# Kernel optimization log

Hardware: AMD Instinct MI355X
Metric: run time of the kernel (lower is better)

## Reference

```python
import jax, jax.numpy as jnp
import numpy as np

EMA_ALPHA = 0.1


def setup_inputs() -> dict:
    key = jax.random.key(0)
    k1, k2, k3 = jax.random.split(key, 3)
    B, N, D = 4, 128, 4096
    T, K = 32768, 8
    memory = jax.random.normal(k1, (B, N, D), dtype=jnp.float32)
    hidden_states = jax.random.normal(k2, (T, D), dtype=jnp.float32)
    slot_indices = jax.random.randint(k3, (T, K), 0, N, dtype=jnp.int64)
    return {
        "memory": memory,
        "hidden_states": hidden_states,
        "slot_indices": slot_indices,
        "batch_idx": 1,
    }


def reference(memory, hidden_states, slot_indices, batch_idx):
    # memory: [B, N, D]; hidden_states: [T, D]; slot_indices: [T, K] int
    N = memory.shape[1]
    # Token t touches slot n if ANY of its top-K indices equals n
    # (mirrors torch (slot_indices == idx).any(dim=-1); duplicates in K count once)
    touch = (slot_indices[..., None] == jnp.arange(N)).any(axis=1)  # [T, N] bool
    m = touch.astype(hidden_states.dtype)                           # [T, N]
    counts = m.sum(axis=0)                                          # [N]
    sums = jnp.einsum("tn,td->nd", m, hidden_states)                # [N, D]
    agg = sums / jnp.maximum(counts, 1.0)[:, None]                  # masked mean per slot
    cur = memory[batch_idx]                                         # [N, D]
    upd = EMA_ALPHA * agg + (1.0 - EMA_ALPHA) * cur
    new_row = jnp.where((counts > 0)[:, None], upd, cur)            # untouched slots unchanged
    return memory.at[batch_idx].set(new_row)
```

## Files before the change

kernel.cpp:

```cpp
#include <hip/hip_runtime.h>
#include <hip/hip_bf16.h>

#define T_TOK   32768
#define N_SLOTS 128
#define D_DIM   4096
#define B_DIM   4

#define NCHUNK  16
#define CTOK    (T_TOK / NCHUNK)
#define KB      64
#define NT      (CTOK / KB)
#define WCOLS   128
#define NSLICE  (D_DIM / WCOLS)
#define THREADS 256

typedef __attribute__((ext_vector_type(8))) short short8;
typedef __attribute__((ext_vector_type(4))) float f32x4;

#define PARTIAL_BYTES ((size_t)NCHUNK * N_SLOTS * D_DIM * 4)
#define COUNTS_OFF    PARTIAL_BYTES

#define BAR_LGKM() do { \
    asm volatile("s_waitcnt lgkmcnt(0)" ::: "memory"); \
    __builtin_amdgcn_s_barrier(); \
  } while (0)

__device__ __forceinline__ unsigned int pack_bf2(float lo, float hi) {
  unsigned short a = __bfloat16_as_ushort(__float2bfloat16(lo));
  unsigned short b = __bfloat16_as_ushort(__float2bfloat16(hi));
  return (unsigned int)a | ((unsigned int)b << 16);
}

__global__ __launch_bounds__(256) void prep_kernel(const int* __restrict__ sidx,
                                                   int* __restrict__ counts) {
  __shared__ int cnt[N_SLOTS];
  const int tid = threadIdx.x;
  if (tid < N_SLOTS) cnt[tid] = 0;
  __syncthreads();

  const int t = blockIdx.x * 256 + tid;
  const int4 a = ((const int4*)sidx)[2 * t];
  const int4 b = ((const int4*)sidx)[2 * t + 1];
  int idx[8] = {a.x, a.y, a.z, a.w, b.x, b.y, b.z, b.w};

  #pragma unroll
  for (int k = 0; k < 8; ++k) {
    int n = idx[k];
    bool dup = false;
    #pragma unroll
    for (int j = 0; j < 8; ++j)
      if (j < k) dup |= (idx[j] == n);
    if (!dup && (unsigned)n < (unsigned)N_SLOTS) atomicAdd(&cnt[n], 1);
  }
  __syncthreads();
  if (tid < N_SLOTS && cnt[tid] > 0) atomicAdd(&counts[tid], cnt[tid]);
}

__global__ __launch_bounds__(THREADS, 2) void sums_kernel(
    const float* __restrict__ hidden, const int* __restrict__ sidx,
    float* __restrict__ partial) {
  __shared__ unsigned int   h_w[2][4096];
  __shared__ unsigned short m_u[2][8192];

  const int tid = threadIdx.x;
  const int slice = blockIdx.x & (NSLICE - 1);
  const int chunk = blockIdx.x / NSLICE;
  const int d0 = slice * WCOLS;
  const int cb = chunk * CTOK;

  const int kp = tid & 31;
  const int cg = tid >> 5;

  const int lane = tid & 63;
  const int wv   = tid >> 6;
  const int l15  = lane & 15;
  const int lk   = lane >> 4;

  f32x4 acc[8][2];
  #pragma unroll
  for (int i = 0; i < 8; ++i)
    #pragma unroll
    for (int j = 0; j < 2; ++j)
      acc[i][j] = (f32x4){0.f, 0.f, 0.f, 0.f};

  float4 fa[4], fb[4];
  int s0, s1;

  {
    const float* hp = hidden + (size_t)(cb + 2 * kp) * D_DIM + d0 + cg * 16;
    #pragma unroll
    for (int q = 0; q < 4; ++q) {
      fa[q] = ((const float4*)hp)[q];
      fb[q] = ((const float4*)(hp + D_DIM))[q];
    }
    s0 = sidx[cb * 8 + tid];
    s1 = sidx[cb * 8 + 256 + tid];
  }

  for (int t = 0; t < NT; ++t) {
    const int b = t & 1;
    const int cs0 = s0, cs1 = s1;

    #pragma unroll
    for (int q = 0; q < 4; ++q) {
      const int colbase = cg * 16 + q * 4;
      const float ax[4] = {fa[q].x, fa[q].y, fa[q].z, fa[q].w};
      const float bx[4] = {fb[q].x, fb[q].y, fb[q].z, fb[q].w};
      #pragma unroll
      for (int c = 0; c < 4; ++c) {
        const int col = colbase + c;
        h_w[b][col * 32 + (kp ^ ((col & 7) << 2))] = pack_bf2(ax[c], bx[c]);
      }
    }

    if (t + 1 < NT) {
      const int tb = cb + (t + 1) * KB;
      const float* hp = hidden + (size_t)(tb + 2 * kp) * D_DIM + d0 + cg * 16;
      #pragma unroll
      for (int q = 0; q < 4; ++q) {
        fa[q] = ((const float4*)hp)[q];
        fb[q] = ((const float4*)(hp + D_DIM))[q];
      }
      s0 = sidx[tb * 8 + tid];
      s1 = sidx[tb * 8 + 256 + tid];
    }

    {
      uint4* mz = (uint4*)m_u[b];
      const uint4 z = make_uint4(0, 0, 0, 0);
      #pragma unroll
      for (int i = 0; i < 4; ++i) mz[i * THREADS + tid] = z;
    }
    BAR_LGKM();

    {
      const int n0 = cs0 & (N_SLOTS - 1);
      const int t0 = tid >> 3;
      m_u[b][n0 * 64 + (t0 ^ ((n0 & 7) << 3))] = 0x3F80;
      const int n1 = cs1 & (N_SLOTS - 1);
      const int t1 = (tid + 256) >> 3;
      m_u[b][n1 * 64 + (t1 ^ ((n1 & 7) << 3))] = 0x3F80;
    }
    BAR_LGKM();

    {
      const unsigned short* mb = m_u[b];
      const unsigned short* hb = (const unsigned short*)h_w[b];
      #pragma unroll
      for (int ks = 0; ks < 2; ++ks) {
        const int kbase = ks * 32 + lk * 8;
        const int col0 = (wv * 2) * 16 + l15;
        const int col1 = (wv * 2 + 1) * 16 + l15;
        const short8 bf0 = *(const short8*)&hb[col0 * 64 + (kbase ^ ((col0 & 7) << 3))];
        const short8 bf1 = *(const short8*)&hb[col1 * 64 + (kbase ^ ((col1 & 7) << 3))];
        #pragma unroll
        for (int mt = 0; mt < 8; ++mt) {
          const int row = mt * 16 + l15;
          const short8 af = *(const short8*)&mb[row * 64 + (kbase ^ ((row & 7) << 3))];
          acc[mt][0] = __builtin_amdgcn_mfma_f32_16x16x32_bf16(af, bf0, acc[mt][0], 0, 0, 0);
          acc[mt][1] = __builtin_amdgcn_mfma_f32_16x16x32_bf16(af, bf1, acc[mt][1], 0, 0, 0);
        }
      }
    }
  }

  float* pbase = partial + (size_t)chunk * N_SLOTS * D_DIM;
  #pragma unroll
  for (int mt = 0; mt < 8; ++mt)
    #pragma unroll
    for (int j = 0; j < 2; ++j) {
      const int col = d0 + (wv * 2 + j) * 16 + l15;
      #pragma unroll
      for (int r = 0; r < 4; ++r) {
        const int row = mt * 16 + lk * 4 + r;
        pbase[(size_t)row * D_DIM + col] = acc[mt][j][r];
      }
    }
}

__global__ __launch_bounds__(256) void final_kernel(const float* __restrict__ memory,
                                                    const float* __restrict__ partial,
                                                    const int* __restrict__ counts,
                                                    const int* __restrict__ bidx_p,
                                                    float* __restrict__ out) {
  const size_t i = (size_t)blockIdx.x * 256 + threadIdx.x;
  float4 v = ((const float4*)memory)[i];
  const size_t rowLen4 = (size_t)N_SLOTS * (D_DIM / 4);
  const size_t rowStart = (size_t)(*bidx_p) * rowLen4;
  if (i >= rowStart && i < rowStart + rowLen4) {
    const size_t rel = i - rowStart;
    const int n  = (int)(rel / (D_DIM / 4));
    const int d4 = (int)(rel % (D_DIM / 4));
    const int c = counts[n];
    if (c > 0) {
      const float4* p4 = (const float4*)partial;
      float4 s = {0.f, 0.f, 0.f, 0.f};
      #pragma unroll
      for (int ch = 0; ch < NCHUNK; ++ch) {
        float4 p = p4[((size_t)ch * N_SLOTS + n) * (D_DIM / 4) + d4];
        s.x += p.x; s.y += p.y; s.z += p.z; s.w += p.w;
      }
      const float w = 0.1f / (float)c;
      v.x = s.x * w + 0.9f * v.x;
      v.y = s.y * w + 0.9f * v.y;
      v.z = s.z * w + 0.9f * v.z;
      v.w = s.w * w + 0.9f * v.w;
    }
  }
  ((float4*)out)[i] = v;
}

extern "C" void kernel_launch(void* const* d_in, const int* in_sizes, int n_in,
                              void* d_out, int out_size, void* d_ws, size_t ws_size,
                              hipStream_t stream) {
  const float* memory = (const float*)d_in[0];
  const float* hidden = (const float*)d_in[1];
  const int*   sidx   = (const int*)d_in[2];
  const int*   bidx   = (const int*)d_in[3];
  float* out = (float*)d_out;

  char* ws = (char*)d_ws;
  float* partial = (float*)ws;
  int*   counts  = (int*)(ws + COUNTS_OFF);

  hipMemsetAsync(counts, 0, 512, stream);

  prep_kernel<<<T_TOK / 256, 256, 0, stream>>>(sidx, counts);

  sums_kernel<<<NCHUNK * NSLICE, THREADS, 0, stream>>>(hidden, sidx, partial);

  const int totalVec4 = B_DIM * N_SLOTS * (D_DIM / 4);
  final_kernel<<<totalVec4 / 256, 256, 0, stream>>>(memory, partial, counts, bidx, out);
}
```

Baseline: 131.7 us.

## Precompute per-token slot bitmaps and build MFMA mask operands in registers

The prep kernel now also writes a 128-bit slot bitmap per token. The sums kernel reads these bitmaps instead of scattering one-hot masks into a zeroed shared-memory matrix, and builds the bf16 mask fragments directly in registers with shifts. This removes one barrier, the mask zeroing and the scatter stores per k-tile. Column slices are halved to 64 columns with more blocks and an occupancy hint of 4, which trades fewer accumulators per thread for more per-lane bit manipulation ALU work and an extra bitmap round trip through global memory.

```diff
diff --git a/kernel.cpp b/kernel.cpp
--- a/kernel.cpp
+++ b/kernel.cpp
@@ -7,18 +7,20 @@
 #define B_DIM   4
 
 #define NCHUNK  16
+#define NSLICE  64
+#define WCOLS   (D_DIM / NSLICE)
 #define CTOK    (T_TOK / NCHUNK)
 #define KB      64
 #define NT      (CTOK / KB)
-#define WCOLS   128
-#define NSLICE  (D_DIM / WCOLS)
 #define THREADS 256
 
+typedef unsigned long long u64;
 typedef __attribute__((ext_vector_type(8))) short short8;
 typedef __attribute__((ext_vector_type(4))) float f32x4;
 
 #define PARTIAL_BYTES ((size_t)NCHUNK * N_SLOTS * D_DIM * 4)
 #define COUNTS_OFF    PARTIAL_BYTES
+#define BITMAP_OFF    (PARTIAL_BYTES + 1024)
 
 #define BAR_LGKM() do { \
     asm volatile("s_waitcnt lgkmcnt(0)" ::: "memory"); \
@@ -32,7 +34,8 @@
 }
 
 __global__ __launch_bounds__(256) void prep_kernel(const int* __restrict__ sidx,
-                                                   int* __restrict__ counts) {
+                                                   int* __restrict__ counts,
+                                                   u64* __restrict__ bitmap) {
   __shared__ int cnt[N_SLOTS];
   const int tid = threadIdx.x;
   if (tid < N_SLOTS) cnt[tid] = 0;
@@ -43,24 +46,29 @@
   const int4 b = ((const int4*)sidx)[2 * t + 1];
   int idx[8] = {a.x, a.y, a.z, a.w, b.x, b.y, b.z, b.w};
 
+  u64 lo = 0, hi = 0;
   #pragma unroll
   for (int k = 0; k < 8; ++k) {
-    int n = idx[k];
+    int n = idx[k] & (N_SLOTS - 1);
+    if (n < 64) lo |= 1ull << n; else hi |= 1ull << (n - 64);
     bool dup = false;
     #pragma unroll
     for (int j = 0; j < 8; ++j)
-      if (j < k) dup |= (idx[j] == n);
-    if (!dup && (unsigned)n < (unsigned)N_SLOTS) atomicAdd(&cnt[n], 1);
-  }
+      if (j < k) dup |= (idx[j] == idx[k]);
+    if (!dup) atomicAdd(&cnt[n], 1);
+  }
+  bitmap[2 * t]     = lo;
+  bitmap[2 * t + 1] = hi;
+
   __syncthreads();
   if (tid < N_SLOTS && cnt[tid] > 0) atomicAdd(&counts[tid], cnt[tid]);
 }
 
-__global__ __launch_bounds__(THREADS, 2) void sums_kernel(
-    const float* __restrict__ hidden, const int* __restrict__ sidx,
+__global__ __launch_bounds__(THREADS, 4) void sums_kernel(
+    const float* __restrict__ hidden, const u64* __restrict__ bitmap,
     float* __restrict__ partial) {
-  __shared__ unsigned int   h_w[2][4096];
-  __shared__ unsigned short m_u[2][8192];
+  __shared__ unsigned int h_w[2][WCOLS * 32];
+  __shared__ __align__(16) u64 mb_w[2][128];
 
   const int tid = threadIdx.x;
   const int slice = blockIdx.x & (NSLICE - 1);
@@ -76,105 +84,93 @@
   const int l15  = lane & 15;
   const int lk   = lane >> 4;
 
-  f32x4 acc[8][2];
+  f32x4 acc[8];
   #pragma unroll
-  for (int i = 0; i < 8; ++i)
-    #pragma unroll
-    for (int j = 0; j < 2; ++j)
-      acc[i][j] = (f32x4){0.f, 0.f, 0.f, 0.f};
-
-  float4 fa[4], fb[4];
-  int s0, s1;
+  for (int mt = 0; mt < 8; ++mt) acc[mt] = (f32x4){0.f, 0.f, 0.f, 0.f};
+
+  float4 fa[2], fb[2];
+  u64 mreg = 0;
 
   {
-    const float* hp = hidden + (size_t)(cb + 2 * kp) * D_DIM + d0 + cg * 16;
-    #pragma unroll
-    for (int q = 0; q < 4; ++q) {
-      fa[q] = ((const float4*)hp)[q];
-      fb[q] = ((const float4*)(hp + D_DIM))[q];
-    }
-    s0 = sidx[cb * 8 + tid];
-    s1 = sidx[cb * 8 + 256 + tid];
+    const float* hp = hidden + (size_t)(cb + 2 * kp) * D_DIM + d0 + cg * 8;
+    fa[0] = ((const float4*)hp)[0];          fa[1] = ((const float4*)hp)[1];
+    fb[0] = ((const float4*)(hp + D_DIM))[0]; fb[1] = ((const float4*)(hp + D_DIM))[1];
+    if (tid < 128) mreg = bitmap[(size_t)cb * 2 + tid];
   }
 
   for (int t = 0; t < NT; ++t) {
     const int b = t & 1;
-    const int cs0 = s0, cs1 = s1;
-
-    #pragma unroll
-    for (int q = 0; q < 4; ++q) {
-      const int colbase = cg * 16 + q * 4;
+
+    #pragma unroll
+    for (int q = 0; q < 2; ++q) {
       const float ax[4] = {fa[q].x, fa[q].y, fa[q].z, fa[q].w};
       const float bx[4] = {fb[q].x, fb[q].y, fb[q].z, fb[q].w};
       #pragma unroll
       for (int c = 0; c < 4; ++c) {
-        const int col = colbase + c;
+        const int col = cg * 8 + q * 4 + c;
         h_w[b][col * 32 + (kp ^ ((col & 7) << 2))] = pack_bf2(ax[c], bx[c]);
       }
     }
+    if (tid < 128) mb_w[b][((tid & 1) << 6) | (tid >> 1)] = mreg;
 
     if (t + 1 < NT) {
       const int tb = cb + (t + 1) * KB;
-      const float* hp = hidden + (size_t)(tb + 2 * kp) * D_DIM + d0 + cg * 16;
-      #pragma unroll
-      for (int q = 0; q < 4; ++q) {
-        fa[q] = ((const float4*)hp)[q];
-        fb[q] = ((const float4*)(hp + D_DIM))[q];
-      }
-      s0 = sidx[tb * 8 + tid];
-      s1 = sidx[tb * 8 + 256 + tid];
-    }
-
-    {
-      uint4* mz = (uint4*)m_u[b];
-      const uint4 z = make_uint4(0, 0, 0, 0);
-      #pragma unroll
-      for (int i = 0; i < 4; ++i) mz[i * THREADS + tid] = z;
-    }
+      const float* hp = hidden + (size_t)(tb + 2 * kp) * D_DIM + d0 + cg * 8;
+      fa[0] = ((const float4*)hp)[0];          fa[1] = ((const float4*)hp)[1];
+      fb[0] = ((const float4*)(hp + D_DIM))[0]; fb[1] = ((const float4*)(hp + D_DIM))[1];
+      if (tid < 128) mreg = bitmap[(size_t)tb * 2 + tid];
+    }
+
     BAR_LGKM();
 
-    {
-      const int n0 = cs0 & (N_SLOTS - 1);
-      const int t0 = tid >> 3;
-      m_u[b][n0 * 64 + (t0 ^ ((n0 & 7) << 3))] = 0x3F80;
-      const int n1 = cs1 & (N_SLOTS - 1);
-      const int t1 = (tid + 256) >> 3;
-      m_u[b][n1 * 64 + (t1 ^ ((n1 & 7) << 3))] = 0x3F80;
-    }
-    BAR_LGKM();
-
-    {
-      const unsigned short* mb = m_u[b];
-      const unsigned short* hb = (const unsigned short*)h_w[b];
-      #pragma unroll
-      for (int ks = 0; ks < 2; ++ks) {
-        const int kbase = ks * 32 + lk * 8;
-        const int col0 = (wv * 2) * 16 + l15;
-        const int col1 = (wv * 2 + 1) * 16 + l15;
-        const short8 bf0 = *(const short8*)&hb[col0 * 64 + (kbase ^ ((col0 & 7) << 3))];
-        const short8 bf1 = *(const short8*)&hb[col1 * 64 + (kbase ^ ((col1 & 7) << 3))];
+    const unsigned short* hb = (const unsigned short*)h_w[b];
+    #pragma unroll
+    for (int ks = 0; ks < 2; ++ks) {
+      const int kbase = ks * 32 + lk * 8;
+      const int col = wv * 16 + l15;
+      const short8 bf = *(const short8*)&hb[col * 64 + (kbase ^ ((col & 7) << 3))];
+
+      u64 w0[8], w1[8];
+      #pragma unroll
+      for (int g = 0; g < 4; ++g) {
+        const ulonglong2 r0 = *(const ulonglong2*)&mb_w[b][kbase + 2 * g];
+        w0[2 * g] = r0.x; w0[2 * g + 1] = r0.y;
+        const ulonglong2 r1 = *(const ulonglong2*)&mb_w[b][64 + kbase + 2 * g];
+        w1[2 * g] = r1.x; w1[2 * g + 1] = r1.y;
+      }
+      unsigned int a0[8], a1[8], c0[8], c1[8];
+      #pragma unroll
+      for (int j = 0; j < 8; ++j) {
+        const u64 s0 = w0[j] >> l15;
+        a0[j] = (unsigned int)s0; a1[j] = (unsigned int)(s0 >> 32);
+        const u64 s1 = w1[j] >> l15;
+        c0[j] = (unsigned int)s1; c1[j] = (unsigned int)(s1 >> 32);
+      }
+      #pragma unroll
+      for (int mt = 0; mt < 8; ++mt) {
+        const unsigned int* src = (mt < 4) ? ((mt & 2) ? a1 : a0)
+                                           : ((mt & 2) ? c1 : c0);
+        const int sh = (mt & 1) * 16;
+        union { unsigned int u[4]; short8 s; } cv;
         #pragma unroll
-        for (int mt = 0; mt < 8; ++mt) {
-          const int row = mt * 16 + l15;
-          const short8 af = *(const short8*)&mb[row * 64 + (kbase ^ ((row & 7) << 3))];
-          acc[mt][0] = __builtin_amdgcn_mfma_f32_16x16x32_bf16(af, bf0, acc[mt][0], 0, 0, 0);
-          acc[mt][1] = __builtin_amdgcn_mfma_f32_16x16x32_bf16(af, bf1, acc[mt][1], 0, 0, 0);
+        for (int p = 0; p < 4; ++p) {
+          const unsigned int b0 = (src[2 * p]     >> sh) & 1u;
+          const unsigned int b1 = (src[2 * p + 1] >> sh) & 1u;
+          cv.u[p] = (b0 | (b1 << 16)) * 0x3F80u;
         }
+        acc[mt] = __builtin_amdgcn_mfma_f32_16x16x32_bf16(cv.s, bf, acc[mt], 0, 0, 0);
       }
     }
   }
 
   float* pbase = partial + (size_t)chunk * N_SLOTS * D_DIM;
+  const int col = d0 + wv * 16 + l15;
   #pragma unroll
   for (int mt = 0; mt < 8; ++mt)
     #pragma unroll
-    for (int j = 0; j < 2; ++j) {
-      const int col = d0 + (wv * 2 + j) * 16 + l15;
-      #pragma unroll
-      for (int r = 0; r < 4; ++r) {
-        const int row = mt * 16 + lk * 4 + r;
-        pbase[(size_t)row * D_DIM + col] = acc[mt][j][r];
-      }
+    for (int r = 0; r < 4; ++r) {
+      const int row = mt * 16 + lk * 4 + r;
+      pbase[(size_t)row * D_DIM + col] = acc[mt][r];
     }
 }
 
@@ -222,12 +218,13 @@
   char* ws = (char*)d_ws;
   float* partial = (float*)ws;
   int*   counts  = (int*)(ws + COUNTS_OFF);
+  u64*   bitmap  = (u64*)(ws + BITMAP_OFF);
 
   hipMemsetAsync(counts, 0, 512, stream);
 
-  prep_kernel<<<T_TOK / 256, 256, 0, stream>>>(sidx, counts);
-
-  sums_kernel<<<NCHUNK * NSLICE, THREADS, 0, stream>>>(hidden, sidx, partial);
+  prep_kernel<<<T_TOK / 256, 256, 0, stream>>>(sidx, counts, bitmap);
+
+  sums_kernel<<<NCHUNK * NSLICE, THREADS, 0, stream>>>(hidden, bitmap, partial);
 
   const int totalVec4 = B_DIM * N_SLOTS * (D_DIM / 4);
   final_kernel<<<totalVec4 / 256, 256, 0, stream>>>(memory, partial, counts, bidx, out);
```

New measurement: 151.4 us. +15.0%, slower.

## Shrink sums-kernel tiles to 64 columns and 32-token steps for higher occupancy

Applied to the files above, without the earlier changes.

The sums kernel now splits D into 64 slices of 64 columns and steps through 32 tokens per iteration, so it launches twice as many blocks. Launch bounds now ask for 4 blocks per CU, and each thread holds 8 accumulators instead of 16. The XOR-swizzled shared layout is replaced by padded rows (stride 40 bf16) to avoid bank conflicts. This is meant to raise occupancy and parallelism. In exchange there are twice as many barrier iterations per chunk, less MFMA work between barriers, and the mask tile is rebuilt twice as often relative to compute.

```diff
diff --git a/kernel.cpp b/kernel.cpp
--- a/kernel.cpp
+++ b/kernel.cpp
@@ -7,13 +7,15 @@
 #define B_DIM   4
 
 #define NCHUNK  16
+#define NSLICE  64
+#define WCOLS   (D_DIM / NSLICE)
 #define CTOK    (T_TOK / NCHUNK)
-#define KB      64
+#define KB      32
 #define NT      (CTOK / KB)
-#define WCOLS   128
-#define NSLICE  (D_DIM / WCOLS)
 #define THREADS 256
-
+#define PADK    40
+
+typedef unsigned long long u64;
 typedef __attribute__((ext_vector_type(8))) short short8;
 typedef __attribute__((ext_vector_type(4))) float f32x4;
 
@@ -25,10 +27,8 @@
     __builtin_amdgcn_s_barrier(); \
   } while (0)
 
-__device__ __forceinline__ unsigned int pack_bf2(float lo, float hi) {
-  unsigned short a = __bfloat16_as_ushort(__float2bfloat16(lo));
-  unsigned short b = __bfloat16_as_ushort(__float2bfloat16(hi));
-  return (unsigned int)a | ((unsigned int)b << 16);
+__device__ __forceinline__ unsigned short bf16u(float x) {
+  return __bfloat16_as_ushort(__float2bfloat16(x));
 }
 
 __global__ __launch_bounds__(256) void prep_kernel(const int* __restrict__ sidx,
@@ -56,19 +56,19 @@
   if (tid < N_SLOTS && cnt[tid] > 0) atomicAdd(&counts[tid], cnt[tid]);
 }
 
-__global__ __launch_bounds__(THREADS, 2) void sums_kernel(
+__global__ __launch_bounds__(THREADS, 4) void sums_kernel(
     const float* __restrict__ hidden, const int* __restrict__ sidx,
     float* __restrict__ partial) {
-  __shared__ unsigned int   h_w[2][4096];
-  __shared__ unsigned short m_u[2][8192];
+  __shared__ __align__(16) unsigned short h_u[2][WCOLS * PADK];
+  __shared__ __align__(16) unsigned short m_u[2][N_SLOTS * PADK];
 
   const int tid = threadIdx.x;
   const int slice = blockIdx.x & (NSLICE - 1);
-  const int chunk = blockIdx.x / NSLICE;
+  const int chunk = blockIdx.x >> 6;
   const int d0 = slice * WCOLS;
   const int cb = chunk * CTOK;
 
-  const int kp = tid & 31;
+  const int tk = tid & 31;
   const int cg = tid >> 5;
 
   const int lane = tid & 63;
@@ -76,105 +76,72 @@
   const int l15  = lane & 15;
   const int lk   = lane >> 4;
 
-  f32x4 acc[8][2];
+  f32x4 acc[8];
   #pragma unroll
-  for (int i = 0; i < 8; ++i)
-    #pragma unroll
-    for (int j = 0; j < 2; ++j)
-      acc[i][j] = (f32x4){0.f, 0.f, 0.f, 0.f};
-
-  float4 fa[4], fb[4];
-  int s0, s1;
+  for (int mt = 0; mt < 8; ++mt) acc[mt] = (f32x4){0.f, 0.f, 0.f, 0.f};
+
+  float4 fa0, fa1;
+  int s;
 
   {
-    const float* hp = hidden + (size_t)(cb + 2 * kp) * D_DIM + d0 + cg * 16;
-    #pragma unroll
-    for (int q = 0; q < 4; ++q) {
-      fa[q] = ((const float4*)hp)[q];
-      fb[q] = ((const float4*)(hp + D_DIM))[q];
-    }
-    s0 = sidx[cb * 8 + tid];
-    s1 = sidx[cb * 8 + 256 + tid];
+    const float* hp = hidden + (size_t)(cb + tk) * D_DIM + d0 + cg * 8;
+    fa0 = ((const float4*)hp)[0];
+    fa1 = ((const float4*)hp)[1];
+    s = sidx[cb * 8 + tid];
   }
 
   for (int t = 0; t < NT; ++t) {
     const int b = t & 1;
-    const int cs0 = s0, cs1 = s1;
-
-    #pragma unroll
-    for (int q = 0; q < 4; ++q) {
-      const int colbase = cg * 16 + q * 4;
-      const float ax[4] = {fa[q].x, fa[q].y, fa[q].z, fa[q].w};
-      const float bx[4] = {fb[q].x, fb[q].y, fb[q].z, fb[q].w};
-      #pragma unroll
-      for (int c = 0; c < 4; ++c) {
-        const int col = colbase + c;
-        h_w[b][col * 32 + (kp ^ ((col & 7) << 2))] = pack_bf2(ax[c], bx[c]);
+    const float4 ca0 = fa0, ca1 = fa1;
+    const int cs = s;
+
+    {
+      const float v[8] = {ca0.x, ca0.y, ca0.z, ca0.w, ca1.x, ca1.y, ca1.z, ca1.w};
+      #pragma unroll
+      for (int q = 0; q < 8; ++q)
+        h_u[b][(cg * 8 + q) * PADK + tk] = bf16u(v[q]);
+    }
+    {
+      u64* m64 = (u64*)m_u[b];
+      #pragma unroll
+      for (int i = 0; i < 4; ++i) {
+        const int f = i * THREADS + tid;
+        m64[(f >> 3) * (PADK / 4) + (f & 7)] = 0ull;
       }
     }
-
     if (t + 1 < NT) {
       const int tb = cb + (t + 1) * KB;
-      const float* hp = hidden + (size_t)(tb + 2 * kp) * D_DIM + d0 + cg * 16;
-      #pragma unroll
-      for (int q = 0; q < 4; ++q) {
-        fa[q] = ((const float4*)hp)[q];
-        fb[q] = ((const float4*)(hp + D_DIM))[q];
+      const float* hp = hidden + (size_t)(tb + tk) * D_DIM + d0 + cg * 8;
+      fa0 = ((const float4*)hp)[0];
+      fa1 = ((const float4*)hp)[1];
+      s = sidx[tb * 8 + tid];
+    }
+    BAR_LGKM();
+
+    m_u[b][(cs & (N_SLOTS - 1)) * PADK + (tid >> 3)] = 0x3F80;
+    BAR_LGKM();
+
+    {
+      const unsigned short* hb = h_u[b];
+      const unsigned short* mb = m_u[b];
+      const int col = wv * 16 + l15;
+      const short8 bf = *(const short8*)&hb[col * PADK + lk * 8];
+      #pragma unroll
+      for (int mt = 0; mt < 8; ++mt) {
+        const short8 af = *(const short8*)&mb[(mt * 16 + l15) * PADK + lk * 8];
+        acc[mt] = __builtin_amdgcn_mfma_f32_16x16x32_bf16(af, bf, acc[mt], 0, 0, 0);
       }
-      s0 = sidx[tb * 8 + tid];
-      s1 = sidx[tb * 8 + 256 + tid];
-    }
-
-    {
-      uint4* mz = (uint4*)m_u[b];
-      const uint4 z = make_uint4(0, 0, 0, 0);
-      #pragma unroll
-      for (int i = 0; i < 4; ++i) mz[i * THREADS + tid] = z;
-    }
-    BAR_LGKM();
-
-    {
-      const int n0 = cs0 & (N_SLOTS - 1);
-      const int t0 = tid >> 3;
-      m_u[b][n0 * 64 + (t0 ^ ((n0 & 7) << 3))] = 0x3F80;
-      const int n1 = cs1 & (N_SLOTS - 1);
-      const int t1 = (tid + 256) >> 3;
-      m_u[b][n1 * 64 + (t1 ^ ((n1 & 7) << 3))] = 0x3F80;
-    }
-    BAR_LGKM();
-
-    {
-      const unsigned short* mb = m_u[b];
-      const unsigned short* hb = (const unsigned short*)h_w[b];
-      #pragma unroll
-      for (int ks = 0; ks < 2; ++ks) {
-        const int kbase = ks * 32 + lk * 8;
-        const int col0 = (wv * 2) * 16 + l15;
-        const int col1 = (wv * 2 + 1) * 16 + l15;
-        const short8 bf0 = *(const short8*)&hb[col0 * 64 + (kbase ^ ((col0 & 7) << 3))];
-        const short8 bf1 = *(const short8*)&hb[col1 * 64 + (kbase ^ ((col1 & 7) << 3))];
-        #pragma unroll
-        for (int mt = 0; mt < 8; ++mt) {
-          const int row = mt * 16 + l15;
-          const short8 af = *(const short8*)&mb[row * 64 + (kbase ^ ((row & 7) << 3))];
-          acc[mt][0] = __builtin_amdgcn_mfma_f32_16x16x32_bf16(af, bf0, acc[mt][0], 0, 0, 0);
-          acc[mt][1] = __builtin_amdgcn_mfma_f32_16x16x32_bf16(af, bf1, acc[mt][1], 0, 0, 0);
-        }
-      }
     }
   }
 
   float* pbase = partial + (size_t)chunk * N_SLOTS * D_DIM;
+  const int col = d0 + wv * 16 + l15;
   #pragma unroll
   for (int mt = 0; mt < 8; ++mt)
     #pragma unroll
-    for (int j = 0; j < 2; ++j) {
-      const int col = d0 + (wv * 2 + j) * 16 + l15;
-      #pragma unroll
-      for (int r = 0; r < 4; ++r) {
-        const int row = mt * 16 + lk * 4 + r;
-        pbase[(size_t)row * D_DIM + col] = acc[mt][j][r];
-      }
+    for (int r = 0; r < 4; ++r) {
+      const int row = mt * 16 + lk * 4 + r;
+      pbase[(size_t)row * D_DIM + col] = acc[mt][r];
     }
 }
 
@@ -194,17 +161,17 @@
     const int c = counts[n];
     if (c > 0) {
       const float4* p4 = (const float4*)partial;
-      float4 s = {0.f, 0.f, 0.f, 0.f};
+      float4 sum = {0.f, 0.f, 0.f, 0.f};
       #pragma unroll
       for (int ch = 0; ch < NCHUNK; ++ch) {
         float4 p = p4[((size_t)ch * N_SLOTS + n) * (D_DIM / 4) + d4];
-        s.x += p.x; s.y += p.y; s.z += p.z; s.w += p.w;
+        sum.x += p.x; sum.y += p.y; sum.z += p.z; sum.w += p.w;
       }
       const float w = 0.1f / (float)c;
-      v.x = s.x * w + 0.9f * v.x;
-      v.y = s.y * w + 0.9f * v.y;
-      v.z = s.z * w + 0.9f * v.z;
-      v.w = s.w * w + 0.9f * v.w;
+      v.x = sum.x * w + 0.9f * v.x;
+      v.y = sum.y * w + 0.9f * v.y;
+      v.z = sum.z * w + 0.9f * v.z;
+      v.w = sum.w * w + 0.9f * v.w;
     }
   }
   ((float4*)out)[i] = v;
```

New measurement: 163.8 us. 1.24x slower.

## Software-pipeline sums loop with triple-buffered mask and sparse zeroing, one barrier

Applied to the files above, without the earlier changes.

Restructures the main loop of sums_kernel so each iteration writes the current tile's bf16 hidden data and mask entries, then runs MFMA on the previous tile, with a single barrier per iteration instead of two. The mask buffer becomes triple-buffered, and instead of zeroing the whole 16KB mask each tile it clears only the 512 entries set two tiles earlier. The aim is to cut barrier count and LDS zeroing traffic. The costs are an extra 16KB of LDS per block, which may affect the 2-blocks-per-CU occupancy target, and more complex buffer indexing.

```diff
diff --git a/kernel.cpp b/kernel.cpp
--- a/kernel.cpp
+++ b/kernel.cpp
@@ -14,6 +14,7 @@
 #define NSLICE  (D_DIM / WCOLS)
 #define THREADS 256
 
+typedef unsigned long long u64;
 typedef __attribute__((ext_vector_type(8))) short short8;
 typedef __attribute__((ext_vector_type(4))) float f32x4;
 
@@ -60,7 +61,7 @@
     const float* __restrict__ hidden, const int* __restrict__ sidx,
     float* __restrict__ partial) {
   __shared__ unsigned int   h_w[2][4096];
-  __shared__ unsigned short m_u[2][8192];
+  __shared__ unsigned short m_u[3][8192];
 
   const int tid = threadIdx.x;
   const int slice = blockIdx.x & (NSLICE - 1);
@@ -71,6 +72,9 @@
   const int kp = tid & 31;
   const int cg = tid >> 5;
 
+  const int tok0 = tid >> 3;
+  const int tok1 = (tid + 256) >> 3;
+
   const int lane = tid & 63;
   const int wv   = tid >> 6;
   const int l15  = lane & 15;
@@ -83,8 +87,18 @@
     for (int j = 0; j < 2; ++j)
       acc[i][j] = (f32x4){0.f, 0.f, 0.f, 0.f};
 
+  {
+    uint4* mz = (uint4*)&m_u[0][0];
+    const uint4 z = make_uint4(0, 0, 0, 0);
+    #pragma unroll
+    for (int i = 0; i < 12; ++i) mz[i * THREADS + tid] = z;
+  }
+  BAR_LGKM();
+
   float4 fa[4], fb[4];
   int s0, s1;
+  int pv0 = 0, pv1 = 0;
+  int un0 = 0, un1 = 0;
 
   {
     const float* hp = hidden + (size_t)(cb + 2 * kp) * D_DIM + d0 + cg * 16;
@@ -97,9 +111,13 @@
     s1 = sidx[cb * 8 + 256 + tid];
   }
 
+  int mcur = 0;
+
   for (int t = 0; t < NT; ++t) {
-    const int b = t & 1;
+    const int hb = t & 1;
     const int cs0 = s0, cs1 = s1;
+    const int mun = (mcur == 2) ? 0 : mcur + 1;
+    const int mcp = (mun == 2) ? 0 : mun + 1;
 
     #pragma unroll
     for (int q = 0; q < 4; ++q) {
@@ -109,8 +127,14 @@
       #pragma unroll
       for (int c = 0; c < 4; ++c) {
         const int col = colbase + c;
-        h_w[b][col * 32 + (kp ^ ((col & 7) << 2))] = pack_bf2(ax[c], bx[c]);
-      }
+        h_w[hb][col * 32 + (kp ^ ((col & 7) << 2))] = pack_bf2(ax[c], bx[c]);
+      }
+    }
+    {
+      const int n0 = cs0 & (N_SLOTS - 1);
+      m_u[mcur][n0 * 64 + (tok0 ^ ((n0 & 7) << 3))] = 0x3F80;
+      const int n1 = cs1 & (N_SLOTS - 1);
+      m_u[mcur][n1 * 64 + (tok1 ^ ((n1 & 7) << 3))] = 0x3F80;
     }
 
     if (t + 1 < NT) {
@@ -125,34 +149,16 @@
       s1 = sidx[tb * 8 + 256 + tid];
     }
 
-    {
-      uint4* mz = (uint4*)m_u[b];
-      const uint4 z = make_uint4(0, 0, 0, 0);
-      #pragma unroll
-      for (int i = 0; i < 4; ++i) mz[i * THREADS + tid] = z;
-    }
-    BAR_LGKM();
-
-    {
-      const int n0 = cs0 & (N_SLOTS - 1);
-      const int t0 = tid >> 3;
-      m_u[b][n0 * 64 + (t0 ^ ((n0 & 7) << 3))] = 0x3F80;
-      const int n1 = cs1 & (N_SLOTS - 1);
-      const int t1 = (tid + 256) >> 3;
-      m_u[b][n1 * 64 + (t1 ^ ((n1 & 7) << 3))] = 0x3F80;
-    }
-    BAR_LGKM();
-
-    {
-      const unsigned short* mb = m_u[b];
-      const unsigned short* hb = (const unsigned short*)h_w[b];
+    if (t >= 1) {
+      const unsigned short* mb = m_u[mcp];
+      const unsigned short* hb2 = (const unsigned short*)h_w[hb ^ 1];
       #pragma unroll
       for (int ks = 0; ks < 2; ++ks) {
         const int kbase = ks * 32 + lk * 8;
         const int col0 = (wv * 2) * 16 + l15;
         const int col1 = (wv * 2 + 1) * 16 + l15;
-        const short8 bf0 = *(const short8*)&hb[col0 * 64 + (kbase ^ ((col0 & 7) << 3))];
-        const short8 bf1 = *(const short8*)&hb[col1 * 64 + (kbase ^ ((col1 & 7) << 3))];
+        const short8 bf0 = *(const short8*)&hb2[col0 * 64 + (kbase ^ ((col0 & 7) << 3))];
+        const short8 bf1 = *(const short8*)&hb2[col1 * 64 + (kbase ^ ((col1 & 7) << 3))];
         #pragma unroll
         for (int mt = 0; mt < 8; ++mt) {
           const int row = mt * 16 + l15;
@@ -160,6 +166,40 @@
           acc[mt][0] = __builtin_amdgcn_mfma_f32_16x16x32_bf16(af, bf0, acc[mt][0], 0, 0, 0);
           acc[mt][1] = __builtin_amdgcn_mfma_f32_16x16x32_bf16(af, bf1, acc[mt][1], 0, 0, 0);
         }
+      }
+    }
+
+    if (t >= 2) {
+      const int n0 = un0 & (N_SLOTS - 1);
+      m_u[mun][n0 * 64 + (tok0 ^ ((n0 & 7) << 3))] = 0;
+      const int n1 = un1 & (N_SLOTS - 1);
+      m_u[mun][n1 * 64 + (tok1 ^ ((n1 & 7) << 3))] = 0;
+    }
+
+    un0 = pv0; un1 = pv1; pv0 = cs0; pv1 = cs1;
+    mcur = (mcur == 2) ? 0 : mcur + 1;
+
+    BAR_LGKM();
+  }
+
+  {
+    const int mun = (mcur == 2) ? 0 : mcur + 1;
+    const int mcp = (mun == 2) ? 0 : mun + 1;
+    const unsigned short* mb = m_u[mcp];
+    const unsigned short* hb2 = (const unsigned short*)h_w[(NT - 1) & 1];
+    #pragma unroll
+    for (int ks = 0; ks < 2; ++ks) {
+      const int kbase = ks * 32 + lk * 8;
+      const int col0 = (wv * 2) * 16 + l15;
+      const int col1 = (wv * 2 + 1) * 16 + l15;
+      const short8 bf0 = *(const short8*)&hb2[col0 * 64 + (kbase ^ ((col0 & 7) << 3))];
+      const short8 bf1 = *(const short8*)&hb2[col1 * 64 + (kbase ^ ((col1 & 7) << 3))];
+      #pragma unroll
+      for (int mt = 0; mt < 8; ++mt) {
+        const int row = mt * 16 + l15;
+        const short8 af = *(const short8*)&mb[row * 64 + (kbase ^ ((row & 7) << 3))];
+        acc[mt][0] = __builtin_amdgcn_mfma_f32_16x16x32_bf16(af, bf0, acc[mt][0], 0, 0, 0);
+        acc[mt][1] = __builtin_amdgcn_mfma_f32_16x16x32_bf16(af, bf1, acc[mt][1], 0, 0, 0);
       }
     }
   }
```

New measurement: 134.0 us. About the same (+1.8%).
